# Kernel tuning notes

Hardware: AMD Instinct MI355X
Metric: run time of the kernel (lower is better)

## Reference

```python
import jax, jax.numpy as jnp
import numpy as np

EPS = 1e-5
SLOPE = 0.01  # torch F.leaky_relu default


def _group(x, idx):
    # x: (B, C, N), idx: (B, N, K) -> (B, C, N, K)
    return jax.vmap(lambda xb, ib: xb[:, ib])(x, idx)


def _bn_lrelu(y, g, b):
    # BatchNorm2d in training mode: stats over (B, N, K) per channel
    mean = jnp.mean(y, axis=(0, 2, 3), keepdims=True)
    var = jnp.var(y, axis=(0, 2, 3), keepdims=True)
    y = (y - mean) * jax.lax.rsqrt(var + EPS)
    y = y * g[None, :, None, None] + b[None, :, None, None]
    return jnp.where(y >= 0, y, SLOPE * y)


def setup_inputs() -> dict:
    key = jax.random.key(0)
    ks = jax.random.split(key, 12)
    B, N, K, C = 4, 2048, 32, 128
    mlp = [128, 128, 256]
    inp = {
        "pos1": jax.random.normal(ks[0], (B, 3, N), jnp.float32),
        "pos2": jax.random.normal(ks[1], (B, 3, N), jnp.float32),
        "feature1": jax.random.normal(ks[2], (B, C, N), jnp.float32),
        "feature2": jax.random.normal(ks[3], (B, C, N), jnp.float32),
        "idx": jax.random.randint(ks[4], (B, N, K), 0, N, jnp.int32),
    }
    last = 2 * C + 3  # corr_func == 'concat'
    for i, out_c in enumerate(mlp):
        scale = 1.0 / np.sqrt(last)
        inp[f"W{i}"] = jax.random.normal(ks[5 + i], (out_c, last), jnp.float32) * scale
        inp[f"g{i}"] = jnp.ones((out_c,), jnp.float32)
        inp[f"b{i}"] = jnp.zeros((out_c,), jnp.float32)
        last = out_c
    return inp


def reference(pos1, pos2, feature1, feature2, idx,
              W0, g0, b0, W1, g1, b1, W2, g2, b2):
    K = idx.shape[-1]
    pos2_grouped = _group(pos2, idx)               # (B, 3, N, K)
    pos_diff = pos2_grouped - pos1[:, :, :, None]  # (B, 3, N, K)
    feat2_grouped = _group(feature2, idx)          # (B, C, N, K)
    feat1_rep = jnp.broadcast_to(feature1[:, :, :, None],
                                 feature1.shape + (K,))
    x = jnp.concatenate([pos_diff, feat2_grouped, feat1_rep], axis=1)  # (B, 2C+3, N, K)
    for W, g, b in ((W0, g0, b0), (W1, g1, b1), (W2, g2, b2)):
        x = jnp.einsum('bcnk,oc->bonk', x, W)      # 1x1 conv, no bias
        x = _bn_lrelu(x, g, b)
    feat1_new = jnp.max(x, axis=-1)                # max-pool over K neighbors
    return (pos1, feat1_new)
```

## Files before the change

kernel.cpp:

```cpp
#include <hip/hip_runtime.h>
#include <cstdint>

#define BB 4
#define NN 2048
#define KK 32
#define CC 128
#define C0 128
#define C2 256
#define CIN0 259
#define RW 160
#define EPSF 1e-5f
#define SLOPE 0.01f

#define PAR0 0
#define PAR1 256
#define PAR2 512
#define R1OFF 1024
#define MAXOFF 33792
#define MINOFF (MAXOFF + 2097152)
#define PART (MINOFF + 2097152)
#define T2_USH ((PART + 1048576) * 2)
#define T1_USH (T2_USH + BB*NN*RW)
#define WP_USH (T1_USH + BB*NN*RW)

#define NFRAG0 80
#define NFRAG1 32
#define NFRAG2 64

typedef float floatx4 __attribute__((ext_vector_type(4)));
typedef short shortx8 __attribute__((ext_vector_type(8)));

#define MFMA16(A,B,C) __builtin_amdgcn_mfma_f32_16x16x32_bf16((A),(B),(C),0,0,0)

__device__ __forceinline__ ushort f2bf(float f) {
    union { float f; uint u; } v; v.f = f;
    uint r = (v.u + 0x7fffu + ((v.u >> 16) & 1u)) >> 16;
    return (ushort)r;
}

__global__ __launch_bounds__(256) void transpose_fp(const float* __restrict__ feat,
                                                    const float* __restrict__ pos,
                                                    float sign, ushort* __restrict__ dst) {
    __shared__ __align__(16) ushort Ts[32][168];
    int b = blockIdx.x >> 6, n0 = (blockIdx.x & 63) * 32;
    int t = threadIdx.x;
#pragma unroll
    for (int i = 0; i < 16; i++) {
        int c = i * 8 + (t >> 5);
        Ts[t & 31][c] = f2bf(feat[((size_t)b * CC + c) * NN + n0 + (t & 31)]);
    }
    if (t < 96) {
        int c = t >> 5, k = t & 31;
        Ts[k][128 + c] = f2bf(sign * pos[((size_t)b * 3 + c) * NN + n0 + k]);
    }
    if (t < 32) {
        for (int c = 131; c < RW; c++) Ts[t][c] = 0;
    }
    __syncthreads();
    int n = t >> 3, q = t & 7;
    ushort* drow = dst + ((size_t)b * NN + n0 + n) * RW;
    *(uint4*)&drow[q * 16]     = *(const uint4*)&Ts[n][q * 16];
    *(uint4*)&drow[q * 16 + 8] = *(const uint4*)&Ts[n][q * 16 + 8];
    if (q < 4) *(uint4*)&drow[128 + q * 8] = *(const uint4*)&Ts[n][128 + q * 8];
}

__global__ __launch_bounds__(256) void pack_w(const float* __restrict__ W0,
                                              const float* __restrict__ W1,
                                              const float* __restrict__ W2,
                                              short* __restrict__ wp0) {
    int tid = blockIdx.x * 256 + threadIdx.x;
    int fid = tid >> 6, lane = tid & 63, g = (lane >> 4) & 3, lcol = lane & 15;
    short* wp1 = wp0 + NFRAG0 * 512;
    short* wp2 = wp1 + NFRAG1 * 512;
    ushort v[8];
    short* dst;
    if (fid < NFRAG0) {
        int mt = fid / 10, ck = fid % 10, o = mt * 16 + lcol;
        const float* wrow = W0 + (size_t)o * CIN0;
        int gather = (ck < 5);
        int cbase = (gather ? ck : ck - 5) * 32 + g * 8;
#pragma unroll
        for (int i = 0; i < 8; i++) {
            int c = cbase + i;
            float x;
            if (c < 128)      x = gather ? wrow[3 + c] : wrow[131 + c];
            else if (c < 131) x = wrow[c - 128];
            else              x = 0.f;
            v[i] = f2bf(x);
        }
        dst = wp0 + ((size_t)fid * 64 + lane) * 8;
    } else if (fid < NFRAG0 + NFRAG1) {
        int f = fid - NFRAG0, mt = f / 4, ck = f % 4, o = mt * 16 + lcol;
#pragma unroll
        for (int i = 0; i < 8; i++) v[i] = f2bf(W1[(size_t)o * C0 + ck * 32 + g * 8 + i]);
        dst = wp1 + ((size_t)f * 64 + lane) * 8;
    } else {
        int f = fid - NFRAG0 - NFRAG1, mt = f / 4, ck = f % 4, o = mt * 16 + lcol;
#pragma unroll
        for (int i = 0; i < 8; i++) v[i] = f2bf(W2[(size_t)o * C0 + ck * 32 + g * 8 + i]);
        dst = wp2 + ((size_t)f * 64 + lane) * 8;
    }
#pragma unroll
    for (int i = 0; i < 8; i++) dst[i] = (short)v[i];
}

__device__ __forceinline__ void stats128_rows(const floatx4 (&acc)[4][2][2], int wave,
                                              int g, int lcol, int bid, float* ws) {
#pragma unroll
    for (int m = 0; m < 2; m++) {
        floatx4 s = {}, q = {};
#pragma unroll
        for (int p = 0; p < 4; p++)
#pragma unroll
            for (int r = 0; r < 4; r++) {
                float a0 = acc[p][m][0][r], a1 = acc[p][m][1][r];
                s[r] += a0 + a1; q[r] += a0 * a0 + a1 * a1;
            }
#pragma unroll
        for (int r = 0; r < 4; r++) {
            float ss = s[r], qq = q[r];
#pragma unroll
            for (int d = 1; d < 16; d <<= 1) { ss += __shfl_xor(ss, d); qq += __shfl_xor(qq, d); }
            s[r] = ss; q[r] = qq;
        }
        if (lcol == 0) {
            int ch = wave * 32 + m * 16 + g * 4;
            *(floatx4*)&ws[PART + (size_t)bid * 512 + ch] = s;
            *(floatx4*)&ws[PART + (size_t)bid * 512 + 128 + ch] = q;
        }
    }
}

__device__ __forceinline__ void bn_to_H4(const floatx4 (&acc)[4][2][2], int wave, int g,
                                         int lcol, int paroff, const float* __restrict__ ws,
                                         ushort (*H)[32][136]) {
#pragma unroll
    for (int m = 0; m < 2; m++) {
        int ch = wave * 32 + m * 16 + g * 4;
        floatx4 sc = *(const floatx4*)&ws[paroff + ch];
        floatx4 sh = *(const floatx4*)&ws[paroff + 128 + ch];
#pragma unroll
        for (int p = 0; p < 4; p++)
#pragma unroll
            for (int nt = 0; nt < 2; nt++) {
                ushort h[4];
#pragma unroll
                for (int r = 0; r < 4; r++) {
                    float z = fmaf(acc[p][m][nt][r], sc[r], sh[r]);
                    z = z >= 0.f ? z : SLOPE * z;
                    h[r] = f2bf(z);
                }
                uint2 val;
                val.x = (uint)h[0] | ((uint)h[1] << 16);
                val.y = (uint)h[2] | ((uint)h[3] << 16);
                *(uint2*)&H[p][nt * 16 + lcol][ch] = val;
            }
    }
}

template<int NL>
__global__ __launch_bounds__(256, 2) void pass_kernel(
    const ushort* __restrict__ T2x, const ushort* __restrict__ T1x,
    const int* __restrict__ idxg, const short* __restrict__ wp0,
    float* __restrict__ ws)
{
    const int bid = blockIdx.x;
    const int t = threadIdx.x;
    const int wave = t >> 6, lane = t & 63, g = (lane >> 4) & 3, lcol = lane & 15;
    const int pid0 = bid * 4;
    const int b = pid0 >> 11;
    const shortx8* wf0 = (const shortx8*)wp0;
    const shortx8* wf1 = wf0 + NFRAG0 * 64;
    const shortx8* wf2 = wf1 + NFRAG1 * 64;

    const ushort* r0[4]; const ushort* r1[4]; const ushort* fr[4];
#pragma unroll
    for (int p = 0; p < 4; p++) {
        int pid = pid0 + p;
        int n = pid & (NN - 1);
        int j0 = idxg[pid * KK + lcol];
        int j1 = idxg[pid * KK + 16 + lcol];
        r0[p] = T2x + ((size_t)(b * NN + j0)) * RW;
        r1[p] = T2x + ((size_t)(b * NN + j1)) * RW;
        fr[p] = T1x + ((size_t)(b * NN + n)) * RW;
    }

    floatx4 acc[4][2][2] = {};
#pragma unroll
    for (int ck = 0; ck < 5; ck++) {
        shortx8 B0[4], B1[4];
#pragma unroll
        for (int p = 0; p < 4; p++) {
            B0[p] = *(const shortx8*)(r0[p] + ck * 32 + g * 8);
            B1[p] = *(const shortx8*)(r1[p] + ck * 32 + g * 8);
        }
#pragma unroll
        for (int m = 0; m < 2; m++) {
            shortx8 A = wf0[((wave * 2 + m) * 10 + ck) * 64 + lane];
#pragma unroll
            for (int p = 0; p < 4; p++) {
                acc[p][m][0] = MFMA16(A, B0[p], acc[p][m][0]);
                acc[p][m][1] = MFMA16(A, B1[p], acc[p][m][1]);
            }
        }
    }
#pragma unroll
    for (int ck = 0; ck < 5; ck++) {
        shortx8 F[4];
#pragma unroll
        for (int p = 0; p < 4; p++)
            F[p] = *(const shortx8*)(fr[p] + ck * 32 + g * 8);
#pragma unroll
        for (int m = 0; m < 2; m++) {
            shortx8 A = wf0[((wave * 2 + m) * 10 + 5 + ck) * 64 + lane];
#pragma unroll
            for (int p = 0; p < 4; p++) {
                acc[p][m][0] = MFMA16(A, F[p], acc[p][m][0]);
                acc[p][m][1] = MFMA16(A, F[p], acc[p][m][1]);
            }
        }
    }

    if constexpr (NL == 1) {
        stats128_rows(acc, wave, g, lcol, bid, ws);
    } else {
        __shared__ __align__(16) ushort H[4][32][136];
        bn_to_H4(acc, wave, g, lcol, PAR0, ws, H);
        __syncthreads();

        floatx4 acc1[4][2][2] = {};
#pragma unroll
        for (int ck = 0; ck < 4; ck++) {
            shortx8 B0[4], B1[4];
#pragma unroll
            for (int p = 0; p < 4; p++) {
                B0[p] = *(const shortx8*)&H[p][lcol][ck * 32 + g * 8];
                B1[p] = *(const shortx8*)&H[p][lcol + 16][ck * 32 + g * 8];
            }
#pragma unroll
            for (int m = 0; m < 2; m++) {
                shortx8 A = wf1[((wave * 2 + m) * 4 + ck) * 64 + lane];
#pragma unroll
                for (int p = 0; p < 4; p++) {
                    acc1[p][m][0] = MFMA16(A, B0[p], acc1[p][m][0]);
                    acc1[p][m][1] = MFMA16(A, B1[p], acc1[p][m][1]);
                }
            }
        }

        if constexpr (NL == 2) {
            stats128_rows(acc1, wave, g, lcol, bid, ws);
        } else {
            __syncthreads();
            bn_to_H4(acc1, wave, g, lcol, PAR1, ws, H);
            __syncthreads();

#pragma unroll
            for (int mh = 0; mh < 2; mh++) {
                floatx4 acc2[4][2][2] = {};
#pragma unroll
                for (int ck = 0; ck < 4; ck++) {
                    shortx8 B0[4], B1[4];
#pragma unroll
                    for (int p = 0; p < 4; p++) {
                        B0[p] = *(const shortx8*)&H[p][lcol][ck * 32 + g * 8];
                        B1[p] = *(const shortx8*)&H[p][lcol + 16][ck * 32 + g * 8];
                    }
#pragma unroll
                    for (int m = 0; m < 2; m++) {
                        int mt = wave * 4 + mh * 2 + m;
                        shortx8 A = wf2[(mt * 4 + ck) * 64 + lane];
#pragma unroll
                        for (int p = 0; p < 4; p++) {
                            acc2[p][m][0] = MFMA16(A, B0[p], acc2[p][m][0]);
                            acc2[p][m][1] = MFMA16(A, B1[p], acc2[p][m][1]);
                        }
                    }
                }
#pragma unroll
                for (int m = 0; m < 2; m++) {
                    int ch = (wave * 4 + mh * 2 + m) * 16 + g * 4;
                    floatx4 s = {}, q = {};
#pragma unroll
                    for (int p = 0; p < 4; p++)
#pragma unroll
                        for (int r = 0; r < 4; r++) {
                            float a0 = acc2[p][m][0][r], a1 = acc2[p][m][1][r];
                            s[r] += a0 + a1; q[r] += a0 * a0 + a1 * a1;
                        }
#pragma unroll
                    for (int r = 0; r < 4; r++) {
                        float ss = s[r], qq = q[r];
#pragma unroll
                        for (int d = 1; d < 16; d <<= 1) { ss += __shfl_xor(ss, d); qq += __shfl_xor(qq, d); }
                        s[r] = ss; q[r] = qq;
                    }
                    if (lcol == 0) {
                        *(floatx4*)&ws[PART + (size_t)bid * 512 + ch] = s;
                        *(floatx4*)&ws[PART + (size_t)bid * 512 + 256 + ch] = q;
                    }
#pragma unroll
                    for (int p = 0; p < 4; p++) {
                        floatx4 mx, mn;
#pragma unroll
                        for (int r = 0; r < 4; r++) {
                            mx[r] = fmaxf(acc2[p][m][0][r], acc2[p][m][1][r]);
                            mn[r] = fminf(acc2[p][m][0][r], acc2[p][m][1][r]);
                        }
#pragma unroll
                        for (int d = 1; d < 16; d <<= 1) {
#pragma unroll
                            for (int r = 0; r < 4; r++) {
                                mx[r] = fmaxf(mx[r], __shfl_xor(mx[r], d));
                                mn[r] = fminf(mn[r], __shfl_xor(mn[r], d));
                            }
                        }
                        if (lcol == 0) {
                            *(floatx4*)&ws[MAXOFF + (size_t)(pid0 + p) * C2 + ch] = mx;
                            *(floatx4*)&ws[MINOFF + (size_t)(pid0 + p) * C2 + ch] = mn;
                        }
                    }
                }
            }
        }
    }
}

__global__ __launch_bounds__(256) void reduce1(float* __restrict__ ws, int srcoff,
                                               int rows_per_block, int ncol) {
    int j = blockIdx.x, t = threadIdx.x;
    const float* base = ws + srcoff + (size_t)j * rows_per_block * 512;
    float a0 = 0.f, a1 = 0.f;
    for (int i = 0; i < rows_per_block; i++) {
        a0 += base[(size_t)i * 512 + t];
        if (ncol > 256) a1 += base[(size_t)i * 512 + 256 + t];
    }
    ws[R1OFF + (size_t)j * 512 + t] = a0;
    if (ncol > 256) ws[R1OFF + (size_t)j * 512 + 256 + t] = a1;
}

__global__ void finalize(const float* __restrict__ g, const float* __restrict__ bparm,
                         float* __restrict__ ws, int CL, int paroff) {
    int ch = threadIdx.x;
    if (ch >= CL) return;
    float s = 0.f, s2 = 0.f;
    for (int j = 0; j < 64; j++) {
        s  += ws[R1OFF + (size_t)j * 512 + ch];
        s2 += ws[R1OFF + (size_t)j * 512 + CL + ch];
    }
    const float inv = 1.0f / ((float)BB * NN * KK);
    float mean = s * inv, var = s2 * inv - mean * mean;
    float sc = g[ch] * rsqrtf(var + EPSF);
    ws[paroff + ch] = sc;
    ws[paroff + CL + ch] = bparm[ch] - mean * sc;
}

__global__ __launch_bounds__(256) void out_kernel(const float* __restrict__ ws,
                                                  float* __restrict__ out) {
    __shared__ float T[32][261];
    int blk = blockIdx.x;
    int b = blk >> 6, n0 = (blk & 63) * 32;
    int t = threadIdx.x;
    float s = ws[PAR2 + t], sh = ws[PAR2 + C2 + t];
    const float* Mx = ws + MAXOFF;
    const float* Mn = ws + MINOFF;
    for (int r = 0; r < 32; r++) {
        size_t base = ((size_t)(b * NN + n0 + r)) * C2 + t;
        float v = (s >= 0.f) ? Mx[base] : Mn[base];
        float z = fmaf(v, s, sh);
        T[r][t] = z >= 0.f ? z : SLOPE * z;
    }
    __syncthreads();
    float* o2 = out + BB * 3 * NN;
    int c = t & 31, og = t >> 5;
    for (int ss = 0; ss < 32; ss++) {
        int o = og * 32 + ss;
        o2[((size_t)(b * C2 + o)) * NN + n0 + c] = T[c][o];
    }
}

extern "C" void kernel_launch(void* const* d_in, const int* in_sizes, int n_in,
                              void* d_out, int out_size, void* d_ws, size_t ws_size,
                              hipStream_t stream) {
    const float* pos1 = (const float*)d_in[0];
    const float* pos2 = (const float*)d_in[1];
    const float* f1   = (const float*)d_in[2];
    const float* f2   = (const float*)d_in[3];
    const int*   idx  = (const int*)d_in[4];
    const float* W0 = (const float*)d_in[5];
    const float* g0 = (const float*)d_in[6];
    const float* b0 = (const float*)d_in[7];
    const float* W1 = (const float*)d_in[8];
    const float* g1 = (const float*)d_in[9];
    const float* b1 = (const float*)d_in[10];
    const float* W2 = (const float*)d_in[11];
    const float* g2 = (const float*)d_in[12];
    const float* b2 = (const float*)d_in[13];
    float* ws  = (float*)d_ws;
    float* out = (float*)d_out;
    ushort* wsu = (ushort*)d_ws;
    ushort* T2p = wsu + T2_USH;
    ushort* T1p = wsu + T1_USH;
    short* wp0  = (short*)(wsu + WP_USH);

    hipMemcpyAsync(d_out, d_in[0], (size_t)BB * 3 * NN * sizeof(float),
                   hipMemcpyDeviceToDevice, stream);

    transpose_fp<<<BB * 64, 256, 0, stream>>>(f2, pos2,  1.0f, T2p);
    transpose_fp<<<BB * 64, 256, 0, stream>>>(f1, pos1, -1.0f, T1p);
    pack_w<<<(NFRAG0 + NFRAG1 + NFRAG2) * 64 / 256, 256, 0, stream>>>(W0, W1, W2, wp0);

    pass_kernel<1><<<BB * NN / 4, 256, 0, stream>>>(T2p, T1p, idx, wp0, ws);
    reduce1<<<64, 256, 0, stream>>>(ws, PART, 32, 256);
    finalize<<<1, 256, 0, stream>>>(g0, b0, ws, C0, PAR0);

    pass_kernel<2><<<BB * NN / 4, 256, 0, stream>>>(T2p, T1p, idx, wp0, ws);
    reduce1<<<64, 256, 0, stream>>>(ws, PART, 32, 256);
    finalize<<<1, 256, 0, stream>>>(g1, b1, ws, C0, PAR1);

    pass_kernel<3><<<BB * NN / 4, 256, 0, stream>>>(T2p, T1p, idx, wp0, ws);
    reduce1<<<64, 256, 0, stream>>>(ws, PART, 32, 512);
    finalize<<<1, 256, 0, stream>>>(g2, b2, ws, C2, PAR2);

    out_kernel<<<BB * (NN / 32), 256, 0, stream>>>(ws, out);
}
```

Before: 274.8 us.

## Assign one point per wave with swizzled per-wave LDS and no block barriers

Work is split differently. Each wave now owns one query point and computes all output channels, where before four waves shared four points and split the channels. Hidden activations go to a per-wave XOR-swizzled LDS buffer, so block-wide __syncthreads become wave barriers and LDS bank conflicts should drop. Launch bounds move to higher occupancy, and the per-point BN partial sums grow four-fold, so the reduce kernel now reads 128 rows per block. The trade-off is more weight-fragment loads per wave and more partial-stat traffic.

```diff
diff --git a/kernel.cpp b/kernel.cpp
--- a/kernel.cpp
+++ b/kernel.cpp
@@ -19,7 +19,8 @@
 #define MAXOFF 33792
 #define MINOFF (MAXOFF + 2097152)
 #define PART (MINOFF + 2097152)
-#define T2_USH ((PART + 1048576) * 2)
+#define PART_END (PART + 4194304)
+#define T2_USH (PART_END * 2)
 #define T1_USH (T2_USH + BB*NN*RW)
 #define WP_USH (T1_USH + BB*NN*RW)
 
@@ -36,6 +37,10 @@
     union { float f; uint u; } v; v.f = f;
     uint r = (v.u + 0x7fffu + ((v.u >> 16) & 1u)) >> 16;
     return (ushort)r;
+}
+
+__device__ __forceinline__ void* hsw(ushort* Hw, int k, int ch2) {
+    return (void*)((char*)Hw + k * 256 + (ch2 ^ ((k & 7) << 4)));
 }
 
 __global__ __launch_bounds__(256) void transpose_fp(const float* __restrict__ feat,
@@ -104,221 +109,162 @@
     for (int i = 0; i < 8; i++) dst[i] = (short)v[i];
 }
 
-__device__ __forceinline__ void stats128_rows(const floatx4 (&acc)[4][2][2], int wave,
-                                              int g, int lcol, int bid, float* ws) {
-#pragma unroll
-    for (int m = 0; m < 2; m++) {
+template<int NM>
+__device__ __forceinline__ void stats_row(const floatx4 (&acc)[NM][2], int mtbase,
+                                          int g, int lcol, int pid, int sqoff,
+                                          float* __restrict__ ws) {
+#pragma unroll
+    for (int m = 0; m < NM; m++) {
         floatx4 s = {}, q = {};
 #pragma unroll
-        for (int p = 0; p < 4; p++)
-#pragma unroll
-            for (int r = 0; r < 4; r++) {
-                float a0 = acc[p][m][0][r], a1 = acc[p][m][1][r];
-                s[r] += a0 + a1; q[r] += a0 * a0 + a1 * a1;
-            }
-#pragma unroll
         for (int r = 0; r < 4; r++) {
-            float ss = s[r], qq = q[r];
+            float a0 = acc[m][0][r], a1 = acc[m][1][r];
+            float ss = a0 + a1, qq = a0 * a0 + a1 * a1;
 #pragma unroll
             for (int d = 1; d < 16; d <<= 1) { ss += __shfl_xor(ss, d); qq += __shfl_xor(qq, d); }
             s[r] = ss; q[r] = qq;
         }
         if (lcol == 0) {
-            int ch = wave * 32 + m * 16 + g * 4;
-            *(floatx4*)&ws[PART + (size_t)bid * 512 + ch] = s;
-            *(floatx4*)&ws[PART + (size_t)bid * 512 + 128 + ch] = q;
-        }
-    }
-}
-
-__device__ __forceinline__ void bn_to_H4(const floatx4 (&acc)[4][2][2], int wave, int g,
-                                         int lcol, int paroff, const float* __restrict__ ws,
-                                         ushort (*H)[32][136]) {
-#pragma unroll
-    for (int m = 0; m < 2; m++) {
-        int ch = wave * 32 + m * 16 + g * 4;
+            int ch = (mtbase + m) * 16 + g * 4;
+            *(floatx4*)&ws[PART + (size_t)pid * 512 + ch] = s;
+            *(floatx4*)&ws[PART + (size_t)pid * 512 + sqoff + ch] = q;
+        }
+    }
+}
+
+__device__ __forceinline__ void bn_h(const floatx4 (&acc)[8][2], int g, int lcol,
+                                     int paroff, const float* __restrict__ ws,
+                                     ushort* Hw) {
+#pragma unroll
+    for (int mt = 0; mt < 8; mt++) {
+        int ch = mt * 16 + g * 4;
         floatx4 sc = *(const floatx4*)&ws[paroff + ch];
         floatx4 sh = *(const floatx4*)&ws[paroff + 128 + ch];
 #pragma unroll
-        for (int p = 0; p < 4; p++)
-#pragma unroll
-            for (int nt = 0; nt < 2; nt++) {
-                ushort h[4];
-#pragma unroll
-                for (int r = 0; r < 4; r++) {
-                    float z = fmaf(acc[p][m][nt][r], sc[r], sh[r]);
-                    z = z >= 0.f ? z : SLOPE * z;
-                    h[r] = f2bf(z);
-                }
-                uint2 val;
-                val.x = (uint)h[0] | ((uint)h[1] << 16);
-                val.y = (uint)h[2] | ((uint)h[3] << 16);
-                *(uint2*)&H[p][nt * 16 + lcol][ch] = val;
+        for (int nt = 0; nt < 2; nt++) {
+            int k = nt * 16 + lcol;
+            ushort h[4];
+#pragma unroll
+            for (int r = 0; r < 4; r++) {
+                float z = fmaf(acc[mt][nt][r], sc[r], sh[r]);
+                z = fmaxf(z, SLOPE * z);
+                h[r] = f2bf(z);
             }
+            uint2 val;
+            val.x = (uint)h[0] | ((uint)h[1] << 16);
+            val.y = (uint)h[2] | ((uint)h[3] << 16);
+            *(uint2*)hsw(Hw, k, mt * 32 + g * 8) = val;
+        }
     }
 }
 
 template<int NL>
-__global__ __launch_bounds__(256, 2) void pass_kernel(
+__global__ __launch_bounds__(256, (NL == 3 ? 3 : 4)) void pass_kernel(
     const ushort* __restrict__ T2x, const ushort* __restrict__ T1x,
     const int* __restrict__ idxg, const short* __restrict__ wp0,
     float* __restrict__ ws)
 {
-    const int bid = blockIdx.x;
     const int t = threadIdx.x;
-    const int wave = t >> 6, lane = t & 63, g = (lane >> 4) & 3, lcol = lane & 15;
-    const int pid0 = bid * 4;
-    const int b = pid0 >> 11;
+    const int wave = t >> 6, lane = t & 63, g = lane >> 4, lcol = lane & 15;
+    const int pid = blockIdx.x * 4 + wave;
+    const int b = pid >> 11, n = pid & (NN - 1);
     const shortx8* wf0 = (const shortx8*)wp0;
     const shortx8* wf1 = wf0 + NFRAG0 * 64;
     const shortx8* wf2 = wf1 + NFRAG1 * 64;
 
-    const ushort* r0[4]; const ushort* r1[4]; const ushort* fr[4];
-#pragma unroll
-    for (int p = 0; p < 4; p++) {
-        int pid = pid0 + p;
-        int n = pid & (NN - 1);
-        int j0 = idxg[pid * KK + lcol];
-        int j1 = idxg[pid * KK + 16 + lcol];
-        r0[p] = T2x + ((size_t)(b * NN + j0)) * RW;
-        r1[p] = T2x + ((size_t)(b * NN + j1)) * RW;
-        fr[p] = T1x + ((size_t)(b * NN + n)) * RW;
-    }
-
-    floatx4 acc[4][2][2] = {};
+    const int j0 = idxg[pid * KK + lcol];
+    const int j1 = idxg[pid * KK + 16 + lcol];
+    const ushort* r0 = T2x + ((size_t)(b * NN + j0)) * RW;
+    const ushort* r1 = T2x + ((size_t)(b * NN + j1)) * RW;
+    const ushort* fr = T1x + ((size_t)(b * NN + n)) * RW;
+
+    floatx4 acc[8][2] = {};
 #pragma unroll
     for (int ck = 0; ck < 5; ck++) {
-        shortx8 B0[4], B1[4];
-#pragma unroll
-        for (int p = 0; p < 4; p++) {
-            B0[p] = *(const shortx8*)(r0[p] + ck * 32 + g * 8);
-            B1[p] = *(const shortx8*)(r1[p] + ck * 32 + g * 8);
-        }
-#pragma unroll
-        for (int m = 0; m < 2; m++) {
-            shortx8 A = wf0[((wave * 2 + m) * 10 + ck) * 64 + lane];
-#pragma unroll
-            for (int p = 0; p < 4; p++) {
-                acc[p][m][0] = MFMA16(A, B0[p], acc[p][m][0]);
-                acc[p][m][1] = MFMA16(A, B1[p], acc[p][m][1]);
+        shortx8 B0 = *(const shortx8*)(r0 + ck * 32 + g * 8);
+        shortx8 B1 = *(const shortx8*)(r1 + ck * 32 + g * 8);
+#pragma unroll
+        for (int mt = 0; mt < 8; mt++) {
+            shortx8 A = wf0[(mt * 10 + ck) * 64 + lane];
+            acc[mt][0] = MFMA16(A, B0, acc[mt][0]);
+            acc[mt][1] = MFMA16(A, B1, acc[mt][1]);
+        }
+    }
+#pragma unroll
+    for (int ck = 0; ck < 5; ck++) {
+        shortx8 F = *(const shortx8*)(fr + ck * 32 + g * 8);
+#pragma unroll
+        for (int mt = 0; mt < 8; mt++) {
+            shortx8 A = wf0[(mt * 10 + 5 + ck) * 64 + lane];
+            acc[mt][0] = MFMA16(A, F, acc[mt][0]);
+            acc[mt][1] = MFMA16(A, F, acc[mt][1]);
+        }
+    }
+
+    if constexpr (NL == 1) {
+        stats_row<8>(acc, 0, g, lcol, pid, 128, ws);
+    } else {
+        __shared__ __align__(16) ushort Hall[4][4096];
+        ushort* Hw = &Hall[wave][0];
+
+        bn_h(acc, g, lcol, PAR0, ws, Hw);
+        __builtin_amdgcn_wave_barrier();
+
+        floatx4 acc1[8][2] = {};
+#pragma unroll
+        for (int ck = 0; ck < 4; ck++) {
+            shortx8 B0 = *(const shortx8*)hsw(Hw, lcol,      ck * 64 + g * 16);
+            shortx8 B1 = *(const shortx8*)hsw(Hw, lcol + 16, ck * 64 + g * 16);
+#pragma unroll
+            for (int mt = 0; mt < 8; mt++) {
+                shortx8 A = wf1[(mt * 4 + ck) * 64 + lane];
+                acc1[mt][0] = MFMA16(A, B0, acc1[mt][0]);
+                acc1[mt][1] = MFMA16(A, B1, acc1[mt][1]);
             }
         }
-    }
-#pragma unroll
-    for (int ck = 0; ck < 5; ck++) {
-        shortx8 F[4];
-#pragma unroll
-        for (int p = 0; p < 4; p++)
-            F[p] = *(const shortx8*)(fr[p] + ck * 32 + g * 8);
-#pragma unroll
-        for (int m = 0; m < 2; m++) {
-            shortx8 A = wf0[((wave * 2 + m) * 10 + 5 + ck) * 64 + lane];
-#pragma unroll
-            for (int p = 0; p < 4; p++) {
-                acc[p][m][0] = MFMA16(A, F[p], acc[p][m][0]);
-                acc[p][m][1] = MFMA16(A, F[p], acc[p][m][1]);
-            }
-        }
-    }
-
-    if constexpr (NL == 1) {
-        stats128_rows(acc, wave, g, lcol, bid, ws);
-    } else {
-        __shared__ __align__(16) ushort H[4][32][136];
-        bn_to_H4(acc, wave, g, lcol, PAR0, ws, H);
-        __syncthreads();
-
-        floatx4 acc1[4][2][2] = {};
-#pragma unroll
-        for (int ck = 0; ck < 4; ck++) {
-            shortx8 B0[4], B1[4];
-#pragma unroll
-            for (int p = 0; p < 4; p++) {
-                B0[p] = *(const shortx8*)&H[p][lcol][ck * 32 + g * 8];
-                B1[p] = *(const shortx8*)&H[p][lcol + 16][ck * 32 + g * 8];
-            }
-#pragma unroll
-            for (int m = 0; m < 2; m++) {
-                shortx8 A = wf1[((wave * 2 + m) * 4 + ck) * 64 + lane];
-#pragma unroll
-                for (int p = 0; p < 4; p++) {
-                    acc1[p][m][0] = MFMA16(A, B0[p], acc1[p][m][0]);
-                    acc1[p][m][1] = MFMA16(A, B1[p], acc1[p][m][1]);
+
+        if constexpr (NL == 2) {
+            stats_row<8>(acc1, 0, g, lcol, pid, 128, ws);
+        } else {
+            __builtin_amdgcn_wave_barrier();
+            bn_h(acc1, g, lcol, PAR1, ws, Hw);
+            __builtin_amdgcn_wave_barrier();
+
+#pragma unroll
+            for (int mq = 0; mq < 4; mq++) {
+                floatx4 a2[4][2] = {};
+#pragma unroll
+                for (int ck = 0; ck < 4; ck++) {
+                    shortx8 B0 = *(const shortx8*)hsw(Hw, lcol,      ck * 64 + g * 16);
+                    shortx8 B1 = *(const shortx8*)hsw(Hw, lcol + 16, ck * 64 + g * 16);
+#pragma unroll
+                    for (int m = 0; m < 4; m++) {
+                        shortx8 A = wf2[((mq * 4 + m) * 4 + ck) * 64 + lane];
+                        a2[m][0] = MFMA16(A, B0, a2[m][0]);
+                        a2[m][1] = MFMA16(A, B1, a2[m][1]);
+                    }
                 }
-            }
-        }
-
-        if constexpr (NL == 2) {
-            stats128_rows(acc1, wave, g, lcol, bid, ws);
-        } else {
-            __syncthreads();
-            bn_to_H4(acc1, wave, g, lcol, PAR1, ws, H);
-            __syncthreads();
-
-#pragma unroll
-            for (int mh = 0; mh < 2; mh++) {
-                floatx4 acc2[4][2][2] = {};
-#pragma unroll
-                for (int ck = 0; ck < 4; ck++) {
-                    shortx8 B0[4], B1[4];
-#pragma unroll
-                    for (int p = 0; p < 4; p++) {
-                        B0[p] = *(const shortx8*)&H[p][lcol][ck * 32 + g * 8];
-                        B1[p] = *(const shortx8*)&H[p][lcol + 16][ck * 32 + g * 8];
+                stats_row<4>(a2, mq * 4, g, lcol, pid, 256, ws);
+#pragma unroll
+                for (int m = 0; m < 4; m++) {
+                    floatx4 mx, mn;
+#pragma unroll
+                    for (int r = 0; r < 4; r++) {
+                        mx[r] = fmaxf(a2[m][0][r], a2[m][1][r]);
+                        mn[r] = fminf(a2[m][0][r], a2[m][1][r]);
                     }
 #pragma unroll
-                    for (int m = 0; m < 2; m++) {
-                        int mt = wave * 4 + mh * 2 + m;
-                        shortx8 A = wf2[(mt * 4 + ck) * 64 + lane];
-#pragma unroll
-                        for (int p = 0; p < 4; p++) {
-                            acc2[p][m][0] = MFMA16(A, B0[p], acc2[p][m][0]);
-                            acc2[p][m][1] = MFMA16(A, B1[p], acc2[p][m][1]);
+                    for (int d = 1; d < 16; d <<= 1) {
+#pragma unroll
+                        for (int r = 0; r < 4; r++) {
+                            mx[r] = fmaxf(mx[r], __shfl_xor(mx[r], d));
+                            mn[r] = fminf(mn[r], __shfl_xor(mn[r], d));
                         }
                     }
-                }
-#pragma unroll
-                for (int m = 0; m < 2; m++) {
-                    int ch = (wave * 4 + mh * 2 + m) * 16 + g * 4;
-                    floatx4 s = {}, q = {};
-#pragma unroll
-                    for (int p = 0; p < 4; p++)
-#pragma unroll
-                        for (int r = 0; r < 4; r++) {
-                            float a0 = acc2[p][m][0][r], a1 = acc2[p][m][1][r];
-                            s[r] += a0 + a1; q[r] += a0 * a0 + a1 * a1;
-                        }
-#pragma unroll
-                    for (int r = 0; r < 4; r++) {
-                        float ss = s[r], qq = q[r];
-#pragma unroll
-                        for (int d = 1; d < 16; d <<= 1) { ss += __shfl_xor(ss, d); qq += __shfl_xor(qq, d); }
-                        s[r] = ss; q[r] = qq;
-                    }
                     if (lcol == 0) {
-                        *(floatx4*)&ws[PART + (size_t)bid * 512 + ch] = s;
-                        *(floatx4*)&ws[PART + (size_t)bid * 512 + 256 + ch] = q;
-                    }
-#pragma unroll
-                    for (int p = 0; p < 4; p++) {
-                        floatx4 mx, mn;
-#pragma unroll
-                        for (int r = 0; r < 4; r++) {
-                            mx[r] = fmaxf(acc2[p][m][0][r], acc2[p][m][1][r]);
-                            mn[r] = fminf(acc2[p][m][0][r], acc2[p][m][1][r]);
-                        }
-#pragma unroll
-                        for (int d = 1; d < 16; d <<= 1) {
-#pragma unroll
-                            for (int r = 0; r < 4; r++) {
-                                mx[r] = fmaxf(mx[r], __shfl_xor(mx[r], d));
-                                mn[r] = fminf(mn[r], __shfl_xor(mn[r], d));
-                            }
-                        }
-                        if (lcol == 0) {
-                            *(floatx4*)&ws[MAXOFF + (size_t)(pid0 + p) * C2 + ch] = mx;
-                            *(floatx4*)&ws[MINOFF + (size_t)(pid0 + p) * C2 + ch] = mn;
-                        }
+                        int ch = (mq * 4 + m) * 16 + g * 4;
+                        *(floatx4*)&ws[MAXOFF + (size_t)pid * C2 + ch] = mx;
+                        *(floatx4*)&ws[MINOFF + (size_t)pid * C2 + ch] = mn;
                     }
                 }
             }
@@ -411,15 +357,15 @@
     pack_w<<<(NFRAG0 + NFRAG1 + NFRAG2) * 64 / 256, 256, 0, stream>>>(W0, W1, W2, wp0);
 
     pass_kernel<1><<<BB * NN / 4, 256, 0, stream>>>(T2p, T1p, idx, wp0, ws);
-    reduce1<<<64, 256, 0, stream>>>(ws, PART, 32, 256);
+    reduce1<<<64, 256, 0, stream>>>(ws, PART, 128, 256);
     finalize<<<1, 256, 0, stream>>>(g0, b0, ws, C0, PAR0);
 
     pass_kernel<2><<<BB * NN / 4, 256, 0, stream>>>(T2p, T1p, idx, wp0, ws);
-    reduce1<<<64, 256, 0, stream>>>(ws, PART, 32, 256);
+    reduce1<<<64, 256, 0, stream>>>(ws, PART, 128, 256);
     finalize<<<1, 256, 0, stream>>>(g1, b1, ws, C0, PAR1);
 
     pass_kernel<3><<<BB * NN / 4, 256, 0, stream>>>(T2p, T1p, idx, wp0, ws);
-    reduce1<<<64, 256, 0, stream>>>(ws, PART, 32, 512);
+    reduce1<<<64, 256, 0, stream>>>(ws, PART, 128, 512);
     finalize<<<1, 256, 0, stream>>>(g2, b2, ws, C2, PAR2);
 
     out_kernel<<<BB * (NN / 32), 256, 0, stream>>>(ws, out);
```

After: 451.5 us. 1.64x slower.
